# Kernel optimization log

Hardware: AMD Instinct MI355X
Metric: run time of the kernel (lower is better)

## Reference

```python
import jax, jax.numpy as jnp
import numpy as np

NUM_HEADS = 12


def setup_inputs() -> dict:
    key = jax.random.key(0)
    ks = jax.random.split(key, 10)
    B, N, C = 8, 1024, 768
    H = NUM_HEADS
    return {
        "x": jax.random.normal(ks[0], (B, N, C), dtype=jnp.float32),
        "geometric": jax.random.uniform(ks[1], (B, 1, 1, 1), dtype=jnp.float32),
        "text": jax.random.uniform(ks[2], (B, 1, 1, 1), dtype=jnp.float32),
        "color": jax.random.uniform(ks[3], (B, 1, 1, 1), dtype=jnp.float32),
        "W_qkv": jax.random.normal(ks[4], (C, 3 * C), dtype=jnp.float32) * 0.02,
        "W_proj": jax.random.normal(ks[5], (C, C), dtype=jnp.float32) * 0.02,
        "b_proj": jax.random.normal(ks[6], (C,), dtype=jnp.float32) * 0.02,
        "geo_bias": jax.random.normal(ks[7], (1, H, 1, 1), dtype=jnp.float32) * 0.1,
        "txt_bias": jax.random.normal(ks[8], (1, H, 1, 1), dtype=jnp.float32) * 0.1,
        "col_bias": jax.random.normal(ks[9], (1, H, 1, 1), dtype=jnp.float32) * 0.1,
    }


def reference(x, geometric, text, color, W_qkv, W_proj, b_proj, geo_bias, txt_bias, col_bias):
    B, N, C = x.shape
    H = NUM_HEADS
    Dh = C // H
    scale = Dh ** -0.5
    # qkv: [B, N, 3, H, Dh] -> q,k,v each [B, H, N, Dh]
    qkv = (x @ W_qkv).reshape(B, N, 3, H, Dh)
    q = jnp.transpose(qkv[:, :, 0], (0, 2, 1, 3))
    k = jnp.transpose(qkv[:, :, 1], (0, 2, 1, 3))
    v = jnp.transpose(qkv[:, :, 2], (0, 2, 1, 3))
    # scores [B, H, N, N] with additive per-head logo biases
    attn = jnp.einsum("bhnd,bhmd->bhnm", q, k) * scale
    attn = attn + geo_bias * geometric + txt_bias * text + col_bias * color
    attn = jax.nn.softmax(attn, axis=-1)
    out = jnp.einsum("bhnm,bhmd->bhnd", attn, v)  # [B, H, N, Dh]
    out = jnp.transpose(out, (0, 2, 1, 3)).reshape(B, N, C)
    return out @ W_proj + b_proj
```

## Files before the change

kernel.cpp:

```cpp
#include <hip/hip_runtime.h>
#include <hip/hip_bf16.h>


typedef __bf16 b16x8 __attribute__((ext_vector_type(8)));
typedef float f32x4 __attribute__((ext_vector_type(4)));

__device__ __forceinline__ ushort f2b(float f) {
    union { float f; uint u; } v; v.f = f;
    uint u = v.u;
    u += 0x7fffu + ((u >> 16) & 1u);
    return (ushort)(u >> 16);
}

__device__ __forceinline__ uint packbf(float a, float b) {
    union { float f; uint u; } ua, ub; ua.f = a; ub.f = b;
    return ((ua.u + 0x8000u) >> 16) | ((ub.u + 0x8000u) & 0xffff0000u);
}

__device__ __forceinline__ void async_cp16(const void* g, void* l) {
    __builtin_amdgcn_global_load_lds(
        (const __attribute__((address_space(1))) unsigned int*)g,
        (__attribute__((address_space(3))) unsigned int*)l, 16, 0, 0);
}


__global__ void k_conv_x(const float* __restrict__ x, ushort* __restrict__ xb, int n4) {
    int i = blockIdx.x * 256 + threadIdx.x;
    if (i >= n4) return;
    const float4 v = reinterpret_cast<const float4*>(x)[i];
    ushort4 o;
    o.x = f2b(v.x); o.y = f2b(v.y); o.z = f2b(v.z); o.w = f2b(v.w);
    reinterpret_cast<ushort4*>(xb)[i] = o;
}

__global__ __launch_bounds__(256)
void k_transpose_t(const float* __restrict__ W, ushort* __restrict__ Wt, int Nin) {
    __shared__ ushort T[64][65];
    const int k0 = blockIdx.x * 64;
    const int n0 = blockIdx.y * 64;
    const int t  = threadIdx.x;
    const int r  = t >> 4, cg = (t & 15) * 4;
    #pragma unroll
    for (int rr = 0; rr < 64; rr += 16) {
        const float4 v = *reinterpret_cast<const float4*>(&W[(size_t)(k0 + r + rr) * Nin + n0 + cg]);
        T[r + rr][cg + 0] = f2b(v.x); T[r + rr][cg + 1] = f2b(v.y);
        T[r + rr][cg + 2] = f2b(v.z); T[r + rr][cg + 3] = f2b(v.w);
    }
    __syncthreads();
    #pragma unroll
    for (int rr = 0; rr < 64; rr += 16) {
        ushort4 o;
        o.x = T[cg + 0][r + rr]; o.y = T[cg + 1][r + rr];
        o.z = T[cg + 2][r + rr]; o.w = T[cg + 3][r + rr];
        *reinterpret_cast<ushort4*>(&Wt[(size_t)(n0 + r + rr) * 768 + k0 + cg]) = o;
    }
}


template<int MODE>
__global__ __launch_bounds__(256, 2)
void k_gemm(const ushort* __restrict__ A, const ushort* __restrict__ Bt,
            ushort* __restrict__ qo, ushort* __restrict__ ko, ushort* __restrict__ vo,
            float* __restrict__ co, const float* __restrict__ bias,
            int M, int N, int K) {
    __shared__ ushort As[128 * 32];
    __shared__ ushort Bs[128 * 32];
    const int tid  = threadIdx.x;
    const int lane = tid & 63;
    const int w    = tid >> 6;
    const int wm   = w >> 1, wn = w & 1;
    const int m16  = lane & 15, quad = lane >> 4;
    const int mbase = blockIdx.y * 128, nbase = blockIdx.x * 128;

    f32x4 acc[4][4];
    #pragma unroll
    for (int i = 0; i < 4; i++)
        #pragma unroll
        for (int j = 0; j < 4; j++) acc[i][j] = (f32x4){0.f, 0.f, 0.f, 0.f};

    const int rS = w * 32 + (lane >> 2);
    const int cS = (lane & 3) * 8;
    ushort* ldsA0 = &As[(w * 2 + 0) * 512];
    ushort* ldsA1 = &As[(w * 2 + 1) * 512];
    ushort* ldsB0 = &Bs[(w * 2 + 0) * 512];
    ushort* ldsB1 = &Bs[(w * 2 + 1) * 512];
    const ushort* gA0 = &A [(size_t)(mbase + rS)      * K + cS];
    const ushort* gA1 = &A [(size_t)(mbase + rS + 16) * K + cS];
    const ushort* gB0 = &Bt[(size_t)(nbase + rS)      * K + cS];
    const ushort* gB1 = &Bt[(size_t)(nbase + rS + 16) * K + cS];

    for (int kt = 0; kt < K; kt += 32) {
        __syncthreads();
        async_cp16(gA0 + kt, ldsA0);
        async_cp16(gA1 + kt, ldsA1);
        async_cp16(gB0 + kt, ldsB0);
        async_cp16(gB1 + kt, ldsB1);
        __syncthreads();

        b16x8 af[4], bf[4];
        #pragma unroll
        for (int i = 0; i < 4; i++)
            af[i] = *reinterpret_cast<const b16x8*>(&As[(wm * 64 + i * 16 + m16) * 32 + quad * 8]);
        #pragma unroll
        for (int j = 0; j < 4; j++)
            bf[j] = *reinterpret_cast<const b16x8*>(&Bs[(wn * 64 + j * 16 + m16) * 32 + quad * 8]);
        #pragma unroll
        for (int i = 0; i < 4; i++)
            #pragma unroll
            for (int j = 0; j < 4; j++)
                acc[i][j] = __builtin_amdgcn_mfma_f32_16x16x32_bf16(bf[j], af[i], acc[i][j], 0, 0, 0);
    }

    #pragma unroll
    for (int j = 0; j < 4; j++) {
        const int f0 = nbase + wn * 64 + j * 16 + quad * 4;
        #pragma unroll
        for (int i = 0; i < 4; i++) {
            const int tok = mbase + wm * 64 + i * 16 + m16;
            const int b = tok >> 10, n = tok & 1023;
            if (MODE == 0) {
                const int s   = f0 / 768;
                const int rem = f0 - s * 768;
                const int h   = rem >> 6;
                const int d0  = rem & 63;
                if (s < 2) {
                    ushort4 pk;
                    pk.x = f2b(acc[i][j][0]); pk.y = f2b(acc[i][j][1]);
                    pk.z = f2b(acc[i][j][2]); pk.w = f2b(acc[i][j][3]);
                    ushort* base = (s == 0) ? qo : ko;
                    *reinterpret_cast<ushort4*>(
                        &base[((size_t)(b * 12 + h) * 1024 + n) * 64 + d0]) = pk;
                } else {
                    #pragma unroll
                    for (int r = 0; r < 4; r++)
                        vo[((size_t)(b * 12 + h) * 64 + d0 + r) * 1024 + n] =
                            f2b(acc[i][j][r]);
                }
            } else {
                float4 val;
                val.x = acc[i][j][0] + bias[f0 + 0];
                val.y = acc[i][j][1] + bias[f0 + 1];
                val.z = acc[i][j][2] + bias[f0 + 2];
                val.w = acc[i][j][3] + bias[f0 + 3];
                *reinterpret_cast<float4*>(&co[(size_t)tok * N + f0]) = val;
            }
        }
    }
}


#define AP 72

__global__ __launch_bounds__(256)
void k_attn(const ushort* __restrict__ qa, const ushort* __restrict__ ka,
            const ushort* __restrict__ vt, ushort* __restrict__ ao) {
    __shared__ ushort Ks[64 * AP];
    __shared__ ushort Vs[64 * AP];

    const int l    = blockIdx.x;
    const int head = ((l >> 7) * 8) + (l & 7);
    const int qsup = (l >> 3) & 15;
    const int tid  = threadIdx.x;
    const int w    = tid >> 6;
    const int lane = tid & 63;
    const int n    = lane & 15;
    const int q    = lane >> 4;

    const ushort* qh = qa + (size_t)head * 65536;
    const ushort* kh = ka + (size_t)head * 65536;
    const ushort* vh = vt + (size_t)head * 65536;
    const int qrow0 = qsup * 64 + w * 16;

    const b16x8 bq0 = *reinterpret_cast<const b16x8*>(&qh[(qrow0 + n) * 64 + q * 8]);
    const b16x8 bq1 = *reinterpret_cast<const b16x8*>(&qh[(qrow0 + n) * 64 + 32 + q * 8]);

    const int kr0 = tid >> 3, kc0 = (tid & 7) * 8;
    const int kr1 = kr0 + 32, kc1 = kc0;

    int4 kg0, kg1, vg0, vg1;
    kg0 = *reinterpret_cast<const int4*>(&kh[(0 + kr0) * 64 + kc0]);
    kg1 = *reinterpret_cast<const int4*>(&kh[(0 + kr1) * 64 + kc1]);
    vg0 = *reinterpret_cast<const int4*>(&vh[kr0 * 1024 + 0 + kc0]);
    vg1 = *reinterpret_cast<const int4*>(&vh[kr1 * 1024 + 0 + kc1]);

    f32x4 o[4];
    #pragma unroll
    for (int dt = 0; dt < 4; dt++) o[dt] = (f32x4){0, 0, 0, 0};
    float Lacc = 0.f;

    const float SC = 0.125f * 1.4426950408889634f;
    const int s0 = ((q & 1) * 2) * 16 + n;
    const int s1 = s0 + 16;
    const bool lowq = (q < 2);

    for (int m0 = 0; m0 < 1024; m0 += 64) {
        *reinterpret_cast<int4*>(&Ks[kr0 * AP + kc0]) = kg0;
        *reinterpret_cast<int4*>(&Ks[kr1 * AP + kc1]) = kg1;
        *reinterpret_cast<int4*>(&Vs[kr0 * AP + kc0]) = vg0;
        *reinterpret_cast<int4*>(&Vs[kr1 * AP + kc1]) = vg1;
        __syncthreads();

        if (m0 + 64 < 1024) {
            kg0 = *reinterpret_cast<const int4*>(&kh[(m0 + 64 + kr0) * 64 + kc0]);
            kg1 = *reinterpret_cast<const int4*>(&kh[(m0 + 64 + kr1) * 64 + kc1]);
            vg0 = *reinterpret_cast<const int4*>(&vh[kr0 * 1024 + m0 + 64 + kc0]);
            vg1 = *reinterpret_cast<const int4*>(&vh[kr1 * 1024 + m0 + 64 + kc1]);
        }

        #pragma unroll
        for (int mc = 0; mc < 2; mc++) {
            f32x4 st0 = (f32x4){0, 0, 0, 0}, st1 = (f32x4){0, 0, 0, 0};
            {
                const b16x8 a0 = *reinterpret_cast<const b16x8*>(&Ks[(mc * 32 + n) * AP + q * 8]);
                const b16x8 a1 = *reinterpret_cast<const b16x8*>(&Ks[(mc * 32 + n) * AP + 32 + q * 8]);
                st0 = __builtin_amdgcn_mfma_f32_16x16x32_bf16(a0, bq0, st0, 0, 0, 0);
                st0 = __builtin_amdgcn_mfma_f32_16x16x32_bf16(a1, bq1, st0, 0, 0, 0);
            }
            {
                const b16x8 a0 = *reinterpret_cast<const b16x8*>(&Ks[(mc * 32 + 16 + n) * AP + q * 8]);
                const b16x8 a1 = *reinterpret_cast<const b16x8*>(&Ks[(mc * 32 + 16 + n) * AP + 32 + q * 8]);
                st1 = __builtin_amdgcn_mfma_f32_16x16x32_bf16(a0, bq0, st1, 0, 0, 0);
                st1 = __builtin_amdgcn_mfma_f32_16x16x32_bf16(a1, bq1, st1, 0, 0, 0);
            }

            float p00 = __builtin_amdgcn_exp2f(st0[0] * SC);
            float p01 = __builtin_amdgcn_exp2f(st0[1] * SC);
            float p02 = __builtin_amdgcn_exp2f(st0[2] * SC);
            float p03 = __builtin_amdgcn_exp2f(st0[3] * SC);
            float p10 = __builtin_amdgcn_exp2f(st1[0] * SC);
            float p11 = __builtin_amdgcn_exp2f(st1[1] * SC);
            float p12 = __builtin_amdgcn_exp2f(st1[2] * SC);
            float p13 = __builtin_amdgcn_exp2f(st1[3] * SC);
            Lacc += ((p00 + p01) + (p02 + p03)) + ((p10 + p11) + (p12 + p13));

            const uint pk00 = packbf(p00, p01), pk01 = packbf(p02, p03);
            const uint pk10 = packbf(p10, p11), pk11 = packbf(p12, p13);

            uint a, b, dw0, dw1, dw2, dw3;
            a = __shfl((int)pk00, s0); b = __shfl((int)pk10, s0); dw0 = lowq ? a : b;
            a = __shfl((int)pk01, s0); b = __shfl((int)pk11, s0); dw1 = lowq ? a : b;
            a = __shfl((int)pk00, s1); b = __shfl((int)pk10, s1); dw2 = lowq ? a : b;
            a = __shfl((int)pk01, s1); b = __shfl((int)pk11, s1); dw3 = lowq ? a : b;

            union { uint4 u; b16x8 v; } bp;
            bp.u = (uint4){dw0, dw1, dw2, dw3};

            #pragma unroll
            for (int dt = 0; dt < 4; dt++) {
                const b16x8 av = *reinterpret_cast<const b16x8*>(
                    &Vs[(dt * 16 + n) * AP + mc * 32 + q * 8]);
                o[dt] = __builtin_amdgcn_mfma_f32_16x16x32_bf16(av, bp.v, o[dt], 0, 0, 0);
            }
        }
        __syncthreads();
    }

    Lacc += __shfl_xor(Lacc, 16);
    Lacc += __shfl_xor(Lacc, 32);
    const float inv = 1.f / Lacc;

    const int bb = head / 12, h = head - bb * 12;
    ushort* dst = ao + ((size_t)(bb * 1024 + qrow0 + n)) * 768 + h * 64 + q * 4;
    #pragma unroll
    for (int dt = 0; dt < 4; dt++) {
        ushort4 pk;
        pk.x = f2b(o[dt][0] * inv);
        pk.y = f2b(o[dt][1] * inv);
        pk.z = f2b(o[dt][2] * inv);
        pk.w = f2b(o[dt][3] * inv);
        *reinterpret_cast<ushort4*>(dst + dt * 16) = pk;
    }
}


extern "C" void kernel_launch(void* const* d_in, const int* in_sizes, int n_in,
                              void* d_out, int out_size, void* d_ws, size_t ws_size,
                              hipStream_t stream) {
    (void)in_sizes; (void)n_in; (void)out_size; (void)ws_size;
    const float* x     = (const float*)d_in[0];
    const float* Wqkv  = (const float*)d_in[4];
    const float* Wproj = (const float*)d_in[5];
    const float* bproj = (const float*)d_in[6];
    float* out = (float*)d_out;

    char* ws = (char*)d_ws;
    ushort* xb     = (ushort*)ws; ws += (size_t)8192 * 768 * 2;
    ushort* wqkvt  = (ushort*)ws; ws += (size_t)2304 * 768 * 2;
    ushort* wprojt = (ushort*)ws; ws += (size_t)768  * 768 * 2;
    ushort* qa     = (ushort*)ws; ws += (size_t)96 * 1024 * 64 * 2;
    ushort* ka     = (ushort*)ws; ws += (size_t)96 * 1024 * 64 * 2;
    ushort* vt     = (ushort*)ws; ws += (size_t)96 * 64 * 1024 * 2;
    ushort* ao     = (ushort*)ws; ws += (size_t)8192 * 768 * 2;

    k_conv_x<<<dim3(6144), dim3(256), 0, stream>>>(x, xb, 1572864);
    k_transpose_t<<<dim3(12, 36), dim3(256), 0, stream>>>(Wqkv, wqkvt, 2304);
    k_transpose_t<<<dim3(12, 12), dim3(256), 0, stream>>>(Wproj, wprojt, 768);
    k_gemm<0><<<dim3(18, 64), dim3(256), 0, stream>>>(xb, wqkvt, qa, ka, vt,
                                                      nullptr, nullptr, 8192, 2304, 768);
    k_attn<<<dim3(1536), dim3(256), 0, stream>>>(qa, ka, vt, ao);
    k_gemm<1><<<dim3(6, 64), dim3(256), 0, stream>>>(ao, wprojt, nullptr, nullptr, nullptr,
                                                     out, bproj, 8192, 768, 768);
}
```

Before: 230.7 us.

## Process two query tiles per wave in attention and merge prep kernels

```diff
diff --git a/kernel.cpp b/kernel.cpp
--- a/kernel.cpp
+++ b/kernel.cpp
@@ -24,21 +24,30 @@
 }
 
 
-__global__ void k_conv_x(const float* __restrict__ x, ushort* __restrict__ xb, int n4) {
-    int i = blockIdx.x * 256 + threadIdx.x;
-    if (i >= n4) return;
-    const float4 v = reinterpret_cast<const float4*>(x)[i];
-    ushort4 o;
-    o.x = f2b(v.x); o.y = f2b(v.y); o.z = f2b(v.z); o.w = f2b(v.w);
-    reinterpret_cast<ushort4*>(xb)[i] = o;
-}
-
 __global__ __launch_bounds__(256)
-void k_transpose_t(const float* __restrict__ W, ushort* __restrict__ Wt, int Nin) {
+void k_prep(const float* __restrict__ x, ushort* __restrict__ xb,
+            const float* __restrict__ Wqkv, ushort* __restrict__ wqkvt,
+            const float* __restrict__ Wproj, ushort* __restrict__ wprojt) {
     __shared__ ushort T[64][65];
-    const int k0 = blockIdx.x * 64;
-    const int n0 = blockIdx.y * 64;
-    const int t  = threadIdx.x;
+    const int blk = blockIdx.x;
+    const int t   = threadIdx.x;
+
+    if (blk < 6144) {
+        const int i = blk * 256 + t;
+        const float4 v = reinterpret_cast<const float4*>(x)[i];
+        ushort4 o;
+        o.x = f2b(v.x); o.y = f2b(v.y); o.z = f2b(v.z); o.w = f2b(v.w);
+        reinterpret_cast<ushort4*>(xb)[i] = o;
+        return;
+    }
+
+    const bool isqkv = (blk < 6576);
+    const int idx = isqkv ? (blk - 6144) : (blk - 6576);
+    const int Nin = isqkv ? 2304 : 768;
+    const float* W  = isqkv ? Wqkv : Wproj;
+    ushort* Wt      = isqkv ? wqkvt : wprojt;
+    const int k0 = (idx % 12) * 64;
+    const int n0 = (idx / 12) * 64;
     const int r  = t >> 4, cg = (t & 15) * 4;
     #pragma unroll
     for (int rr = 0; rr < 64; rr += 16) {
@@ -158,8 +167,10 @@
     __shared__ ushort Vs[64 * AP];
 
     const int l    = blockIdx.x;
-    const int head = ((l >> 7) * 8) + (l & 7);
-    const int qsup = (l >> 3) & 15;
+    const int xcd  = l & 7;
+    const int g    = l >> 3;
+    const int head = (g % 12) * 8 + xcd;
+    const int qsup = g / 12;
     const int tid  = threadIdx.x;
     const int w    = tid >> 6;
     const int lane = tid & 63;
@@ -169,10 +180,14 @@
     const ushort* qh = qa + (size_t)head * 65536;
     const ushort* kh = ka + (size_t)head * 65536;
     const ushort* vh = vt + (size_t)head * 65536;
-    const int qrow0 = qsup * 64 + w * 16;
-
-    const b16x8 bq0 = *reinterpret_cast<const b16x8*>(&qh[(qrow0 + n) * 64 + q * 8]);
-    const b16x8 bq1 = *reinterpret_cast<const b16x8*>(&qh[(qrow0 + n) * 64 + 32 + q * 8]);
+    const int qrow0 = qsup * 128 + w * 32;
+
+    b16x8 bq0[2], bq1[2];
+    #pragma unroll
+    for (int u = 0; u < 2; u++) {
+        bq0[u] = *reinterpret_cast<const b16x8*>(&qh[(qrow0 + u * 16 + n) * 64 + q * 8]);
+        bq1[u] = *reinterpret_cast<const b16x8*>(&qh[(qrow0 + u * 16 + n) * 64 + 32 + q * 8]);
+    }
 
     const int kr0 = tid >> 3, kc0 = (tid & 7) * 8;
     const int kr1 = kr0 + 32, kc1 = kc0;
@@ -183,10 +198,12 @@
     vg0 = *reinterpret_cast<const int4*>(&vh[kr0 * 1024 + 0 + kc0]);
     vg1 = *reinterpret_cast<const int4*>(&vh[kr1 * 1024 + 0 + kc1]);
 
-    f32x4 o[4];
-    #pragma unroll
-    for (int dt = 0; dt < 4; dt++) o[dt] = (f32x4){0, 0, 0, 0};
-    float Lacc = 0.f;
+    f32x4 o[2][4];
+    #pragma unroll
+    for (int u = 0; u < 2; u++)
+        #pragma unroll
+        for (int dt = 0; dt < 4; dt++) o[u][dt] = (f32x4){0, 0, 0, 0};
+    float Lacc[2] = {0.f, 0.f};
 
     const float SC = 0.125f * 1.4426950408889634f;
     const int s0 = ((q & 1) * 2) * 16 + n;
@@ -209,66 +226,75 @@
 
         #pragma unroll
         for (int mc = 0; mc < 2; mc++) {
-            f32x4 st0 = (f32x4){0, 0, 0, 0}, st1 = (f32x4){0, 0, 0, 0};
-            {
-                const b16x8 a0 = *reinterpret_cast<const b16x8*>(&Ks[(mc * 32 + n) * AP + q * 8]);
-                const b16x8 a1 = *reinterpret_cast<const b16x8*>(&Ks[(mc * 32 + n) * AP + 32 + q * 8]);
-                st0 = __builtin_amdgcn_mfma_f32_16x16x32_bf16(a0, bq0, st0, 0, 0, 0);
-                st0 = __builtin_amdgcn_mfma_f32_16x16x32_bf16(a1, bq1, st0, 0, 0, 0);
+            b16x8 ka0t[2], ka1t[2];
+            #pragma unroll
+            for (int t = 0; t < 2; t++) {
+                ka0t[t] = *reinterpret_cast<const b16x8*>(&Ks[(mc * 32 + t * 16 + n) * AP + q * 8]);
+                ka1t[t] = *reinterpret_cast<const b16x8*>(&Ks[(mc * 32 + t * 16 + n) * AP + 32 + q * 8]);
             }
-            {
-                const b16x8 a0 = *reinterpret_cast<const b16x8*>(&Ks[(mc * 32 + 16 + n) * AP + q * 8]);
-                const b16x8 a1 = *reinterpret_cast<const b16x8*>(&Ks[(mc * 32 + 16 + n) * AP + 32 + q * 8]);
-                st1 = __builtin_amdgcn_mfma_f32_16x16x32_bf16(a0, bq0, st1, 0, 0, 0);
-                st1 = __builtin_amdgcn_mfma_f32_16x16x32_bf16(a1, bq1, st1, 0, 0, 0);
+            f32x4 st[2][2];
+            #pragma unroll
+            for (int u = 0; u < 2; u++)
+                #pragma unroll
+                for (int t = 0; t < 2; t++) {
+                    st[u][t] = (f32x4){0, 0, 0, 0};
+                    st[u][t] = __builtin_amdgcn_mfma_f32_16x16x32_bf16(ka0t[t], bq0[u], st[u][t], 0, 0, 0);
+                    st[u][t] = __builtin_amdgcn_mfma_f32_16x16x32_bf16(ka1t[t], bq1[u], st[u][t], 0, 0, 0);
+                }
+
+            union { uint4 u4; b16x8 v; } bp[2];
+            #pragma unroll
+            for (int u = 0; u < 2; u++) {
+                float p00 = __builtin_amdgcn_exp2f(st[u][0][0] * SC);
+                float p01 = __builtin_amdgcn_exp2f(st[u][0][1] * SC);
+                float p02 = __builtin_amdgcn_exp2f(st[u][0][2] * SC);
+                float p03 = __builtin_amdgcn_exp2f(st[u][0][3] * SC);
+                float p10 = __builtin_amdgcn_exp2f(st[u][1][0] * SC);
+                float p11 = __builtin_amdgcn_exp2f(st[u][1][1] * SC);
+                float p12 = __builtin_amdgcn_exp2f(st[u][1][2] * SC);
+                float p13 = __builtin_amdgcn_exp2f(st[u][1][3] * SC);
+                Lacc[u] += ((p00 + p01) + (p02 + p03)) + ((p10 + p11) + (p12 + p13));
+
+                const uint pk00 = packbf(p00, p01), pk01 = packbf(p02, p03);
+                const uint pk10 = packbf(p10, p11), pk11 = packbf(p12, p13);
+
+                uint a, b, dw0, dw1, dw2, dw3;
+                a = __shfl((int)pk00, s0); b = __shfl((int)pk10, s0); dw0 = lowq ? a : b;
+                a = __shfl((int)pk01, s0); b = __shfl((int)pk11, s0); dw1 = lowq ? a : b;
+                a = __shfl((int)pk00, s1); b = __shfl((int)pk10, s1); dw2 = lowq ? a : b;
+                a = __shfl((int)pk01, s1); b = __shfl((int)pk11, s1); dw3 = lowq ? a : b;
+                bp[u].u4 = (uint4){dw0, dw1, dw2, dw3};
             }
-
-            float p00 = __builtin_amdgcn_exp2f(st0[0] * SC);
-            float p01 = __builtin_amdgcn_exp2f(st0[1] * SC);
-            float p02 = __builtin_amdgcn_exp2f(st0[2] * SC);
-            float p03 = __builtin_amdgcn_exp2f(st0[3] * SC);
-            float p10 = __builtin_amdgcn_exp2f(st1[0] * SC);
-            float p11 = __builtin_amdgcn_exp2f(st1[1] * SC);
-            float p12 = __builtin_amdgcn_exp2f(st1[2] * SC);
-            float p13 = __builtin_amdgcn_exp2f(st1[3] * SC);
-            Lacc += ((p00 + p01) + (p02 + p03)) + ((p10 + p11) + (p12 + p13));
-
-            const uint pk00 = packbf(p00, p01), pk01 = packbf(p02, p03);
-            const uint pk10 = packbf(p10, p11), pk11 = packbf(p12, p13);
-
-            uint a, b, dw0, dw1, dw2, dw3;
-            a = __shfl((int)pk00, s0); b = __shfl((int)pk10, s0); dw0 = lowq ? a : b;
-            a = __shfl((int)pk01, s0); b = __shfl((int)pk11, s0); dw1 = lowq ? a : b;
-            a = __shfl((int)pk00, s1); b = __shfl((int)pk10, s1); dw2 = lowq ? a : b;
-            a = __shfl((int)pk01, s1); b = __shfl((int)pk11, s1); dw3 = lowq ? a : b;
-
-            union { uint4 u; b16x8 v; } bp;
-            bp.u = (uint4){dw0, dw1, dw2, dw3};
 
             #pragma unroll
             for (int dt = 0; dt < 4; dt++) {
                 const b16x8 av = *reinterpret_cast<const b16x8*>(
                     &Vs[(dt * 16 + n) * AP + mc * 32 + q * 8]);
-                o[dt] = __builtin_amdgcn_mfma_f32_16x16x32_bf16(av, bp.v, o[dt], 0, 0, 0);
+                #pragma unroll
+                for (int u = 0; u < 2; u++)
+                    o[u][dt] = __builtin_amdgcn_mfma_f32_16x16x32_bf16(av, bp[u].v, o[u][dt], 0, 0, 0);
             }
         }
         __syncthreads();
     }
 
-    Lacc += __shfl_xor(Lacc, 16);
-    Lacc += __shfl_xor(Lacc, 32);
-    const float inv = 1.f / Lacc;
-
     const int bb = head / 12, h = head - bb * 12;
-    ushort* dst = ao + ((size_t)(bb * 1024 + qrow0 + n)) * 768 + h * 64 + q * 4;
-    #pragma unroll
-    for (int dt = 0; dt < 4; dt++) {
-        ushort4 pk;
-        pk.x = f2b(o[dt][0] * inv);
-        pk.y = f2b(o[dt][1] * inv);
-        pk.z = f2b(o[dt][2] * inv);
-        pk.w = f2b(o[dt][3] * inv);
-        *reinterpret_cast<ushort4*>(dst + dt * 16) = pk;
+    #pragma unroll
+    for (int u = 0; u < 2; u++) {
+        float L = Lacc[u];
+        L += __shfl_xor(L, 16);
+        L += __shfl_xor(L, 32);
+        const float inv = 1.f / L;
+        ushort* dst = ao + ((size_t)(bb * 1024 + qrow0 + u * 16 + n)) * 768 + h * 64 + q * 4;
+        #pragma unroll
+        for (int dt = 0; dt < 4; dt++) {
+            ushort4 pk;
+            pk.x = f2b(o[u][dt][0] * inv);
+            pk.y = f2b(o[u][dt][1] * inv);
+            pk.z = f2b(o[u][dt][2] * inv);
+            pk.w = f2b(o[u][dt][3] * inv);
+            *reinterpret_cast<ushort4*>(dst + dt * 16) = pk;
+        }
     }
 }
 
@@ -292,12 +318,10 @@
     ushort* vt     = (ushort*)ws; ws += (size_t)96 * 64 * 1024 * 2;
     ushort* ao     = (ushort*)ws; ws += (size_t)8192 * 768 * 2;
 
-    k_conv_x<<<dim3(6144), dim3(256), 0, stream>>>(x, xb, 1572864);
-    k_transpose_t<<<dim3(12, 36), dim3(256), 0, stream>>>(Wqkv, wqkvt, 2304);
-    k_transpose_t<<<dim3(12, 12), dim3(256), 0, stream>>>(Wproj, wprojt, 768);
+    k_prep<<<dim3(6720), dim3(256), 0, stream>>>(x, xb, Wqkv, wqkvt, Wproj, wprojt);
     k_gemm<0><<<dim3(18, 64), dim3(256), 0, stream>>>(xb, wqkvt, qa, ka, vt,
                                                       nullptr, nullptr, 8192, 2304, 768);
-    k_attn<<<dim3(1536), dim3(256), 0, stream>>>(qa, ka, vt, ao);
+    k_attn<<<dim3(768), dim3(256), 0, stream>>>(qa, ka, vt, ao);
     k_gemm<1><<<dim3(6, 64), dim3(256), 0, stream>>>(ao, wprojt, nullptr, nullptr, nullptr,
                                                      out, bproj, 8192, 768, 768);
 }
```

After: 217.6 us. 1.06x faster.
